# Kernel optimization log

Hardware: AMD Instinct MI355X
Metric: run time of the kernel (lower is better)

## Reference

```python
import jax, jax.numpy as jnp
import numpy as np

DIM = 32          # image/vq dim (ImageTransform3D default dim=32 == vq.layers[0].dim)
CODEBOOK = 1024   # number of codebook entries
TOTAL = 4194304   # flat weight-vector length (multiple of DIM)


def setup_inputs() -> dict:
    key = jax.random.key(0)
    k1, k2, k3 = jax.random.split(key, 3)
    weights = jax.random.normal(k1, (TOTAL,), dtype=jnp.float32)
    condition = jax.random.normal(k2, (1, DIM, TOTAL // DIM), dtype=jnp.float32)
    codebook = jax.random.normal(k3, (CODEBOOK, DIM), dtype=jnp.float32)
    return {"weights": weights, "condition": condition, "codebook": codebook}


def reference(weights, condition, codebook):
    # --- ImageTransform3D.forward: pad flat weights to a multiple of DIM, view (1, DIM, -1)
    pad = (-weights.shape[0]) % DIM  # static
    if pad:
        weights = jnp.concatenate([weights, jnp.zeros((pad,), weights.dtype)])
    img = weights.reshape(1, DIM, -1)
    # --- TokenTransform3D: subtract condition, flatten to tokens of size DIM
    x = (img - condition).reshape(-1, DIM)  # [N, DIM]
    # --- VectorQuantize (freeze_codebook, eval): nearest-neighbour lookup
    d = (
        jnp.sum(x * x, axis=-1, keepdims=True)
        - 2.0 * (x @ codebook.T)
        + jnp.sum(codebook * codebook, axis=-1)
    )
    indices = jnp.argmin(d, axis=-1)  # [N] int32
    return indices
```

## Files before the change

kernel.cpp:

```cpp
#include <hip/hip_runtime.h>

#define TOTAL     4194304
#define DIM       32
#define NTOK      (TOTAL / DIM)
#define NCODE     1024
#define DELTA_EPS 2e-3f
#define FLAGBIT   0x40000000

typedef _Float16 half8   __attribute__((ext_vector_type(8)));
typedef float    floatx4 __attribute__((ext_vector_type(4)));

#define GLOAD_LDS16(g, l) \
    __builtin_amdgcn_global_load_lds((const __attribute__((address_space(1))) void*)(g), \
                                     (__attribute__((address_space(3))) void*)(l), 16, 0, 0)
#define GLOAD_LDS4(g, l) \
    __builtin_amdgcn_global_load_lds((const __attribute__((address_space(1))) void*)(g), \
                                     (__attribute__((address_space(3))) void*)(l), 4, 0, 0)

__global__ __launch_bounds__(64) void vq_prep(
    const float* __restrict__ cb, float* __restrict__ nhb,
    _Float16* __restrict__ Eh, _Float16* __restrict__ El)
{
    const int k = blockIdx.x * 64 + threadIdx.x;
    const float4* e4 = reinterpret_cast<const float4*>(cb) + (size_t)k * 8;
    float v[DIM];
    float4 t[8];
#pragma unroll
    for (int j = 0; j < 8; ++j) t[j] = e4[j];
#pragma unroll
    for (int j = 0; j < 8; ++j) {
        v[4 * j + 0] = t[j].x; v[4 * j + 1] = t[j].y;
        v[4 * j + 2] = t[j].z; v[4 * j + 3] = t[j].w;
    }
    float e2 = 0.0f;
#pragma unroll
    for (int i = 0; i < DIM; ++i) e2 = fmaf(v[i], v[i], e2);
    nhb[k] = -0.5f * e2;

    const int gs = k >> 4, l15 = k & 15;
#pragma unroll
    for (int l4 = 0; l4 < 4; ++l4) {
        half8 h, lo;
#pragma unroll
        for (int j = 0; j < 8; ++j) {
            float x = v[l4 * 8 + j];
            _Float16 hh = (_Float16)x;
            h[j]  = hh;
            lo[j] = (_Float16)(x - (float)hh);
        }
        const int slot = gs * 64 + l4 * 16 + l15;
        *reinterpret_cast<half8*>(Eh + (size_t)slot * 8) = h;
        *reinterpret_cast<half8*>(El + (size_t)slot * 8) = lo;
    }
}

__global__ __launch_bounds__(1024) void vq_main(
    const float* __restrict__ w, const float* __restrict__ c,
    const float* __restrict__ nhb, const _Float16* __restrict__ Eh,
    const _Float16* __restrict__ El, const float* __restrict__ cb,
    int* __restrict__ out)
{
    __shared__ _Float16 sEh[4096 * 8];
    __shared__ _Float16 sEl[4096 * 8];
    __shared__ float    snh[NCODE];
    __shared__ int      sOut[512];

    const int tid  = threadIdx.x;
    const int lane = tid & 63;
    const int wid  = tid >> 6;
    const int tokw = blockIdx.x * 512 + wid * 32;
    const int l15  = lane & 15;
    const int l4   = lane >> 4;

    half8 xh[2], xl[2];
#pragma unroll
    for (int m = 0; m < 2; ++m) {
        const int token = tokw + m * 16 + l15;
        const float4* pw = reinterpret_cast<const float4*>(w + (size_t)token * DIM + l4 * 8);
        const float4* pc = reinterpret_cast<const float4*>(c + (size_t)token * DIM + l4 * 8);
        float4 a0 = pw[0], a1 = pw[1], b0 = pc[0], b1 = pc[1];
        float xs[8] = {a0.x - b0.x, a0.y - b0.y, a0.z - b0.z, a0.w - b0.w,
                       a1.x - b1.x, a1.y - b1.y, a1.z - b1.z, a1.w - b1.w};
#pragma unroll
        for (int j = 0; j < 8; ++j) {
            _Float16 h = (_Float16)xs[j];
            xh[m][j] = h;
            xl[m][j] = (_Float16)(xs[j] - (float)h);
        }
    }

    {
#pragma unroll
        for (int r = 0; r < 4; ++r) {
            const int slot = r * 1024 + wid * 64;
            GLOAD_LDS16(Eh + (size_t)(slot + lane) * 8, sEh + (size_t)slot * 8);
            GLOAD_LDS16(El + (size_t)(slot + lane) * 8, sEl + (size_t)slot * 8);
        }
        GLOAD_LDS4(nhb + wid * 64 + lane, snh + wid * 64);
    }
    __syncthreads();

    const float NEGINF = __uint_as_float(0xFF800000u);
    float best[8], second[8];
#pragma unroll
    for (int q = 0; q < 8; ++q) { best[q] = NEGINF; second[q] = NEGINF; }

#pragma unroll 4
    for (int sp = 0; sp < 32; ++sp) {
        const int sA = 2 * sp, sB = 2 * sp + 1;
        const half8 ehA = *reinterpret_cast<const half8*>(sEh + (size_t)(sA * 64 + lane) * 8);
        const half8 elA = *reinterpret_cast<const half8*>(sEl + (size_t)(sA * 64 + lane) * 8);
        const half8 ehB = *reinterpret_cast<const half8*>(sEh + (size_t)(sB * 64 + lane) * 8);
        const half8 elB = *reinterpret_cast<const half8*>(sEl + (size_t)(sB * 64 + lane) * 8);
        const float nhA = snh[sA * 16 + l15];
        const float nhB = snh[sB * 16 + l15];
        const unsigned ixA = 1023u - (unsigned)(sA * 16 + l15);
        const unsigned ixB = ixA - 16u;
        const floatx4 nA = {nhA, nhA, nhA, nhA};
        const floatx4 nB = {nhB, nhB, nhB, nhB};
#pragma unroll
        for (int m = 0; m < 2; ++m) {
            floatx4 aA = __builtin_amdgcn_mfma_f32_16x16x32_f16(xh[m], ehA, nA, 0, 0, 0);
            aA = __builtin_amdgcn_mfma_f32_16x16x32_f16(xl[m], ehA, aA, 0, 0, 0);
            aA = __builtin_amdgcn_mfma_f32_16x16x32_f16(xh[m], elA, aA, 0, 0, 0);
            floatx4 aB = __builtin_amdgcn_mfma_f32_16x16x32_f16(xh[m], ehB, nB, 0, 0, 0);
            aB = __builtin_amdgcn_mfma_f32_16x16x32_f16(xl[m], ehB, aB, 0, 0, 0);
            aB = __builtin_amdgcn_mfma_f32_16x16x32_f16(xh[m], elB, aB, 0, 0, 0);
#pragma unroll
            for (int r = 0; r < 4; ++r) {
                const int q = m * 4 + r;
                float pA = __uint_as_float((__float_as_uint(aA[r]) & 0xFFFFFC00u) | ixA);
                float pB = __uint_as_float((__float_as_uint(aB[r]) & 0xFFFFFC00u) | ixB);
                second[q] = fmaxf(second[q], __builtin_amdgcn_fmed3f(pA, pB, best[q]));
                best[q]   = fmaxf(fmaxf(best[q], pA), pB);
            }
        }
    }

#pragma unroll
    for (int sh = 1; sh < 16; sh <<= 1) {
#pragma unroll
        for (int q = 0; q < 8; ++q) {
            float bB = __shfl_xor(best[q], sh);
            float sB = __shfl_xor(second[q], sh);
            second[q] = fmaxf(fmaxf(second[q], sB), fminf(best[q], bB));
            best[q]   = fmaxf(best[q], bB);
        }
    }

    if (l15 == 0) {
#pragma unroll
        for (int m = 0; m < 2; ++m) {
#pragma unroll
            for (int r = 0; r < 4; ++r) {
                const int q = m * 4 + r;
                unsigned ub = __float_as_uint(best[q]);
                unsigned us = __float_as_uint(second[q]);
                float bv = __uint_as_float(ub & 0xFFFFFC00u);
                float sv = __uint_as_float(us & 0xFFFFFC00u);
                int eb = (int)((ub >> 23) & 255u);
                int es = (int)((us >> 23) & 255u);
                int em = eb > es ? eb : es;
                em = em > 12 ? em : 12;
                float thr = __uint_as_float((unsigned)(em - 11) << 23) + DELTA_EPS;
                int k = 1023 - (int)(ub & 1023u);
                sOut[wid * 32 + m * 16 + l4 * 4 + r] = ((bv - sv) < thr) ? (k | FLAGBIT) : k;
            }
        }
    }

    int myval = 0;
    if (lane < 32) myval = sOut[wid * 32 + lane];
    unsigned long long mask = __ballot(lane < 32 && (myval & FLAGBIT));
    while (mask) {
        const int src = __ffsll(mask) - 1;
        mask &= mask - 1;
        const int token = tokw + src;

        float x[DIM];
#pragma unroll
        for (int j = 0; j < 8; ++j) {
            float4 aw = reinterpret_cast<const float4*>(w + (size_t)token * DIM)[j];
            float4 ac = reinterpret_cast<const float4*>(c + (size_t)token * DIM)[j];
            x[4 * j + 0] = aw.x - ac.x; x[4 * j + 1] = aw.y - ac.y;
            x[4 * j + 2] = aw.z - ac.z; x[4 * j + 3] = aw.w - ac.w;
        }
        float x2 = 0.f;
#pragma unroll
        for (int i = 0; i < DIM; ++i) x2 = fmaf(x[i], x[i], x2);

        float dmin = INFINITY;
        int   kbest = 0;
#pragma unroll 2
        for (int i = 0; i < 16; ++i) {
            const int k = lane + 64 * i;
            const float4* e4 = reinterpret_cast<const float4*>(cb) + (size_t)k * 8;
            float4 ev[8];
#pragma unroll
            for (int j = 0; j < 8; ++j) ev[j] = e4[j];
            float dot = 0.f;
#pragma unroll
            for (int j = 0; j < 8; ++j) {
                dot = fmaf(x[4 * j + 0], ev[j].x, dot);
                dot = fmaf(x[4 * j + 1], ev[j].y, dot);
                dot = fmaf(x[4 * j + 2], ev[j].z, dot);
                dot = fmaf(x[4 * j + 3], ev[j].w, dot);
            }
            float e2 = -2.0f * nhb[k];
            float dd = fmaf(-2.0f, dot, x2) + e2;
            if (dd < dmin) { dmin = dd; kbest = k; }
        }
#pragma unroll
        for (int sh = 1; sh < 64; sh <<= 1) {
            float dB = __shfl_xor(dmin, sh);
            int   iB = __shfl_xor(kbest, sh);
            bool take = (dB < dmin) || (dB == dmin && iB < kbest);
            dmin = take ? dB : dmin;
            kbest = take ? iB : kbest;
        }
        if (lane == src) myval = kbest;
    }
    if (lane < 32) out[tokw + lane] = myval;
}

extern "C" void kernel_launch(void* const* d_in, const int* in_sizes, int n_in,
                              void* d_out, int out_size, void* d_ws, size_t ws_size,
                              hipStream_t stream) {
    const float* w  = (const float*)d_in[0];
    const float* c  = (const float*)d_in[1];
    const float* cb = (const float*)d_in[2];
    int* out = (int*)d_out;

    char* wsb = (char*)d_ws;
    float*    nhb = (float*)wsb;
    _Float16* Eh  = (_Float16*)(wsb + 4096);
    _Float16* El  = (_Float16*)(wsb + 4096 + 65536);

    vq_prep<<<NCODE / 64, 64, 0, stream>>>(cb, nhb, Eh, El);
    vq_main<<<NTOK / 512, 1024, 0, stream>>>(w, c, nhb, Eh, El, cb, out);
}
```

Measured before the change: 53.01 us.

## Keep codebook slices in registers and stream token tiles from LDS

Swaps the operand roles in the main loop. Each wave now holds a fixed 64-entry slice of the codebook (high and low fp16 halves plus norms) in registers. It loops over 32 token tiles that are staged in shared memory, instead of holding tokens in registers and streaming the full codebook from LDS. Per-wave partial best and second-best values go to an LDS buffer and are merged across the 16 waves in a new reduction pass before the flagging step. This cuts the LDS footprint and per-iteration LDS reads, at the cost of an extra barrier, partial-result traffic and a shuffle reduction for every tile rather than once per wave.

```diff
diff --git a/kernel.cpp b/kernel.cpp
--- a/kernel.cpp
+++ b/kernel.cpp
@@ -9,13 +9,6 @@
 
 typedef _Float16 half8   __attribute__((ext_vector_type(8)));
 typedef float    floatx4 __attribute__((ext_vector_type(4)));
-
-#define GLOAD_LDS16(g, l) \
-    __builtin_amdgcn_global_load_lds((const __attribute__((address_space(1))) void*)(g), \
-                                     (__attribute__((address_space(3))) void*)(l), 16, 0, 0)
-#define GLOAD_LDS4(g, l) \
-    __builtin_amdgcn_global_load_lds((const __attribute__((address_space(1))) void*)(g), \
-                                     (__attribute__((address_space(3))) void*)(l), 4, 0, 0)
 
 __global__ __launch_bounds__(64) void vq_prep(
     const float* __restrict__ cb, float* __restrict__ nhb,
@@ -60,115 +53,137 @@
     const _Float16* __restrict__ El, const float* __restrict__ cb,
     int* __restrict__ out)
 {
-    __shared__ _Float16 sEh[4096 * 8];
-    __shared__ _Float16 sEl[4096 * 8];
-    __shared__ float    snh[NCODE];
+    __shared__ _Float16 sXh[2048 * 8];
+    __shared__ _Float16 sXl[2048 * 8];
+    __shared__ float2   sPart[16 * 512];
     __shared__ int      sOut[512];
 
     const int tid  = threadIdx.x;
     const int lane = tid & 63;
     const int wid  = tid >> 6;
-    const int tokw = blockIdx.x * 512 + wid * 32;
+    const int tok0 = blockIdx.x * 512;
     const int l15  = lane & 15;
     const int l4   = lane >> 4;
 
-    half8 xh[2], xl[2];
-#pragma unroll
-    for (int m = 0; m < 2; ++m) {
-        const int token = tokw + m * 16 + l15;
-        const float4* pw = reinterpret_cast<const float4*>(w + (size_t)token * DIM + l4 * 8);
-        const float4* pc = reinterpret_cast<const float4*>(c + (size_t)token * DIM + l4 * 8);
-        float4 a0 = pw[0], a1 = pw[1], b0 = pc[0], b1 = pc[1];
-        float xs[8] = {a0.x - b0.x, a0.y - b0.y, a0.z - b0.z, a0.w - b0.w,
-                       a1.x - b1.x, a1.y - b1.y, a1.z - b1.z, a1.w - b1.w};
-#pragma unroll
-        for (int j = 0; j < 8; ++j) {
-            _Float16 h = (_Float16)xs[j];
-            xh[m][j] = h;
-            xl[m][j] = (_Float16)(xs[j] - (float)h);
-        }
+    half8 beh[4], bel[4];
+    float bnh[4];
+    unsigned bix[4];
+#pragma unroll
+    for (int s = 0; s < 4; ++s) {
+        const int gs = wid * 4 + s;
+        beh[s] = *reinterpret_cast<const half8*>(Eh + (size_t)(gs * 64 + lane) * 8);
+        bel[s] = *reinterpret_cast<const half8*>(El + (size_t)(gs * 64 + lane) * 8);
+        bnh[s] = nhb[gs * 16 + l15];
+        bix[s] = 1023u - (unsigned)(gs * 16 + l15);
     }
 
     {
-#pragma unroll
-        for (int r = 0; r < 4; ++r) {
-            const int slot = r * 1024 + wid * 64;
-            GLOAD_LDS16(Eh + (size_t)(slot + lane) * 8, sEh + (size_t)slot * 8);
-            GLOAD_LDS16(El + (size_t)(slot + lane) * 8, sEl + (size_t)slot * 8);
-        }
-        GLOAD_LDS4(nhb + wid * 64 + lane, snh + wid * 64);
+        const int t    = tid >> 1;
+        const int half = tid & 1;
+        const int token = tok0 + t;
+        const float4* pw = reinterpret_cast<const float4*>(w + (size_t)token * DIM + half * 16);
+        const float4* pc = reinterpret_cast<const float4*>(c + (size_t)token * DIM + half * 16);
+        float4 a0 = pw[0], a1 = pw[1], a2 = pw[2], a3 = pw[3];
+        float4 b0 = pc[0], b1 = pc[1], b2 = pc[2], b3 = pc[3];
+        float xs[16] = {a0.x - b0.x, a0.y - b0.y, a0.z - b0.z, a0.w - b0.w,
+                        a1.x - b1.x, a1.y - b1.y, a1.z - b1.z, a1.w - b1.w,
+                        a2.x - b2.x, a2.y - b2.y, a2.z - b2.z, a2.w - b2.w,
+                        a3.x - b3.x, a3.y - b3.y, a3.z - b3.z, a3.w - b3.w};
+        const int tile = t >> 4, row = t & 15;
+#pragma unroll
+        for (int qq = 0; qq < 2; ++qq) {
+            half8 h, lo;
+#pragma unroll
+            for (int j = 0; j < 8; ++j) {
+                float x = xs[qq * 8 + j];
+                _Float16 hh = (_Float16)x;
+                h[j]  = hh;
+                lo[j] = (_Float16)(x - (float)hh);
+            }
+            const int q = half * 2 + qq;
+            const int slot = tile * 64 + q * 16 + row;
+            *reinterpret_cast<half8*>(sXh + (size_t)slot * 8) = h;
+            *reinterpret_cast<half8*>(sXl + (size_t)slot * 8) = lo;
+        }
     }
     __syncthreads();
 
     const float NEGINF = __uint_as_float(0xFF800000u);
-    float best[8], second[8];
-#pragma unroll
-    for (int q = 0; q < 8; ++q) { best[q] = NEGINF; second[q] = NEGINF; }
 
 #pragma unroll 4
-    for (int sp = 0; sp < 32; ++sp) {
-        const int sA = 2 * sp, sB = 2 * sp + 1;
-        const half8 ehA = *reinterpret_cast<const half8*>(sEh + (size_t)(sA * 64 + lane) * 8);
-        const half8 elA = *reinterpret_cast<const half8*>(sEl + (size_t)(sA * 64 + lane) * 8);
-        const half8 ehB = *reinterpret_cast<const half8*>(sEh + (size_t)(sB * 64 + lane) * 8);
-        const half8 elB = *reinterpret_cast<const half8*>(sEl + (size_t)(sB * 64 + lane) * 8);
-        const float nhA = snh[sA * 16 + l15];
-        const float nhB = snh[sB * 16 + l15];
-        const unsigned ixA = 1023u - (unsigned)(sA * 16 + l15);
-        const unsigned ixB = ixA - 16u;
-        const floatx4 nA = {nhA, nhA, nhA, nhA};
-        const floatx4 nB = {nhB, nhB, nhB, nhB};
-#pragma unroll
-        for (int m = 0; m < 2; ++m) {
-            floatx4 aA = __builtin_amdgcn_mfma_f32_16x16x32_f16(xh[m], ehA, nA, 0, 0, 0);
-            aA = __builtin_amdgcn_mfma_f32_16x16x32_f16(xl[m], ehA, aA, 0, 0, 0);
-            aA = __builtin_amdgcn_mfma_f32_16x16x32_f16(xh[m], elA, aA, 0, 0, 0);
-            floatx4 aB = __builtin_amdgcn_mfma_f32_16x16x32_f16(xh[m], ehB, nB, 0, 0, 0);
-            aB = __builtin_amdgcn_mfma_f32_16x16x32_f16(xl[m], ehB, aB, 0, 0, 0);
-            aB = __builtin_amdgcn_mfma_f32_16x16x32_f16(xh[m], elB, aB, 0, 0, 0);
+    for (int tt = 0; tt < 32; ++tt) {
+        const int tile = (tt + wid * 2) & 31;
+        const half8 xh = *reinterpret_cast<const half8*>(sXh + (size_t)(tile * 64 + lane) * 8);
+        const half8 xl = *reinterpret_cast<const half8*>(sXl + (size_t)(tile * 64 + lane) * 8);
+
+        float bb[4], ss[4];
+#pragma unroll
+        for (int r = 0; r < 4; ++r) { bb[r] = NEGINF; ss[r] = NEGINF; }
+
+#pragma unroll
+        for (int sp = 0; sp < 2; ++sp) {
+            const int s0 = 2 * sp, s1 = 2 * sp + 1;
+            const floatx4 n0 = {bnh[s0], bnh[s0], bnh[s0], bnh[s0]};
+            const floatx4 n1 = {bnh[s1], bnh[s1], bnh[s1], bnh[s1]};
+            floatx4 aA = __builtin_amdgcn_mfma_f32_16x16x32_f16(xh, beh[s0], n0, 0, 0, 0);
+            aA = __builtin_amdgcn_mfma_f32_16x16x32_f16(xl, beh[s0], aA, 0, 0, 0);
+            aA = __builtin_amdgcn_mfma_f32_16x16x32_f16(xh, bel[s0], aA, 0, 0, 0);
+            floatx4 aB = __builtin_amdgcn_mfma_f32_16x16x32_f16(xh, beh[s1], n1, 0, 0, 0);
+            aB = __builtin_amdgcn_mfma_f32_16x16x32_f16(xl, beh[s1], aB, 0, 0, 0);
+            aB = __builtin_amdgcn_mfma_f32_16x16x32_f16(xh, bel[s1], aB, 0, 0, 0);
 #pragma unroll
             for (int r = 0; r < 4; ++r) {
-                const int q = m * 4 + r;
-                float pA = __uint_as_float((__float_as_uint(aA[r]) & 0xFFFFFC00u) | ixA);
-                float pB = __uint_as_float((__float_as_uint(aB[r]) & 0xFFFFFC00u) | ixB);
-                second[q] = fmaxf(second[q], __builtin_amdgcn_fmed3f(pA, pB, best[q]));
-                best[q]   = fmaxf(fmaxf(best[q], pA), pB);
-            }
-        }
-    }
-
-#pragma unroll
-    for (int sh = 1; sh < 16; sh <<= 1) {
-#pragma unroll
-        for (int q = 0; q < 8; ++q) {
-            float bB = __shfl_xor(best[q], sh);
-            float sB = __shfl_xor(second[q], sh);
-            second[q] = fmaxf(fmaxf(second[q], sB), fminf(best[q], bB));
-            best[q]   = fmaxf(best[q], bB);
-        }
-    }
-
-    if (l15 == 0) {
-#pragma unroll
-        for (int m = 0; m < 2; ++m) {
+                float pA = __uint_as_float((__float_as_uint(aA[r]) & 0xFFFFFC00u) | bix[s0]);
+                float pB = __uint_as_float((__float_as_uint(aB[r]) & 0xFFFFFC00u) | bix[s1]);
+                ss[r] = fmaxf(ss[r], __builtin_amdgcn_fmed3f(pA, pB, bb[r]));
+                bb[r] = fmaxf(fmaxf(bb[r], pA), pB);
+            }
+        }
+
+#pragma unroll
+        for (int sh = 1; sh < 16; sh <<= 1) {
 #pragma unroll
             for (int r = 0; r < 4; ++r) {
-                const int q = m * 4 + r;
-                unsigned ub = __float_as_uint(best[q]);
-                unsigned us = __float_as_uint(second[q]);
-                float bv = __uint_as_float(ub & 0xFFFFFC00u);
-                float sv = __uint_as_float(us & 0xFFFFFC00u);
-                int eb = (int)((ub >> 23) & 255u);
-                int es = (int)((us >> 23) & 255u);
-                int em = eb > es ? eb : es;
-                em = em > 12 ? em : 12;
-                float thr = __uint_as_float((unsigned)(em - 11) << 23) + DELTA_EPS;
-                int k = 1023 - (int)(ub & 1023u);
-                sOut[wid * 32 + m * 16 + l4 * 4 + r] = ((bv - sv) < thr) ? (k | FLAGBIT) : k;
-            }
-        }
-    }
-
+                float bB = __shfl_xor(bb[r], sh);
+                float sB = __shfl_xor(ss[r], sh);
+                ss[r] = fmaxf(fmaxf(ss[r], sB), fminf(bb[r], bB));
+                bb[r] = fmaxf(bb[r], bB);
+            }
+        }
+        if (l15 == 0) {
+#pragma unroll
+            for (int r = 0; r < 4; ++r) {
+                const int trow = tile * 16 + l4 * 4 + r;
+                sPart[wid * 512 + trow] = make_float2(bb[r], ss[r]);
+            }
+        }
+    }
+    __syncthreads();
+
+    if (tid < 512) {
+        float best = NEGINF, second = NEGINF;
+#pragma unroll
+        for (int p = 0; p < 16; ++p) {
+            float2 v = sPart[p * 512 + tid];
+            float nb = fmaxf(best, v.x);
+            second = fmaxf(fmaxf(second, v.y), fminf(best, v.x));
+            best = nb;
+        }
+        unsigned ub = __float_as_uint(best);
+        unsigned us = __float_as_uint(second);
+        float bv = __uint_as_float(ub & 0xFFFFFC00u);
+        float sv = __uint_as_float(us & 0xFFFFFC00u);
+        int eb = (int)((ub >> 23) & 255u);
+        int es = (int)((us >> 23) & 255u);
+        int em = eb > es ? eb : es;
+        em = em > 12 ? em : 12;
+        float thr = __uint_as_float((unsigned)(em - 11) << 23) + DELTA_EPS;
+        int k = 1023 - (int)(ub & 1023u);
+        sOut[tid] = ((bv - sv) < thr) ? (k | FLAGBIT) : k;
+    }
+    __syncthreads();
+
+    const int tokw = tok0 + wid * 32;
     int myval = 0;
     if (lane < 32) myval = sOut[wid * 32 + lane];
     unsigned long long mask = __ballot(lane < 32 && (myval & FLAGBIT));
```

Measured after the change: 93.29 us. 1.76x slower.
